# Performance work log

Measured on AMD Instinct MI355X. Metric: run time of the kernel, lower is better.

Reference implementation:

```python
import jax, jax.numpy as jnp
import numpy as np

B, L, Z, G = 512, 2713, 58, 8  # batch, chem features, seq len (zeta), d_model (gamma)
H, HD, FF, NL = 8, 1, 2048, 6  # heads, head_dim, ffn dim, layers
RNA_IN, LIN1, LIN2 = 1018, 256, 64
CAT, C1, C2 = LIN2 + Z * G, 64, 8  # 528, 64, 8


def setup_inputs() -> dict:
    key = jax.random.key(0)
    ks = iter(jax.random.split(key, 40))
    r = lambda shape, s=0.05: (jax.random.normal(next(ks), shape, dtype=jnp.float32) * s)
    inp = {
        'rna': jax.random.normal(next(ks), (B, RNA_IN), dtype=jnp.float32),
        'drug': jax.random.normal(next(ks), (B, L, Z), dtype=jnp.float32),
        'lin1_w': r((LIN1, RNA_IN)), 'lin1_b': r((LIN1,)),
        'lin2_w': r((LIN2, LIN1)), 'lin2_b': r((LIN2,)),
        'chem_w': r((G, L)),  # chem_embedding: Linear(2713->8, no bias)
        'pos_w': r((G, Z)),   # pos_embedding on one-hot == its weight columns
        'qkv_w': r((NL, 3 * G, G)), 'qkv_b': r((NL, 3 * G)),
        'out_w': r((NL, G, G)), 'out_b': r((NL, G)),
        'ln1_g': jnp.ones((NL, G), jnp.float32), 'ln1_b': jnp.zeros((NL, G), jnp.float32),
        'ff1_w': r((NL, FF, G)), 'ff1_b': r((NL, FF)),
        'ff2_w': r((NL, G, FF)), 'ff2_b': r((NL, G)),
        'ln2_g': jnp.ones((NL, G), jnp.float32), 'ln2_b': jnp.zeros((NL, G), jnp.float32),
        'c1_w': r((C1, CAT)), 'c1_b': r((C1,)),
        'c2_w': r((C2, C1)), 'c2_b': r((C2,)),
        'c3_w': r((1, C2)), 'c3_b': r((1,)),
    }
    return inp


def _layernorm(x, g, b, eps=1e-5):
    mu = jnp.mean(x, axis=-1, keepdims=True)
    var = jnp.mean(jnp.square(x - mu), axis=-1, keepdims=True)
    return (x - mu) * jax.lax.rsqrt(var + eps) * g + b


def _forward(rna, drug, lin1_w, lin1_b, lin2_w, lin2_b, chem_w, pos_w,
             qkv_w, qkv_b, out_w, out_b, ln1_g, ln1_b,
             ff1_w, ff1_b, ff2_w, ff2_b, ln2_g, ln2_b,
             c1_w, c1_b, c2_w, c2_b, c3_w, c3_b):
    # rna branch: two linear layers (no activation in original forward)
    r = rna @ lin1_w.T + lin1_b
    r = r @ lin2_w.T + lin2_b  # [B, 64]

    # Embedding: E = W_chem @ M + W_pos (the double loop, vectorized)
    E = jnp.einsum('gl,blz->bgz', chem_w, drug) + pos_w[None]  # [B, G, Z]
    x = jnp.transpose(E, (0, 2, 1))  # [B, Z, G] (batch_first transformer input)

    scale = 1.0 / np.sqrt(HD)
    for i in range(NL):  # 6 post-norm TransformerEncoderLayers, relu FFN
        qkv = x @ qkv_w[i].T + qkv_b[i]  # [B, Z, 3G]
        q, k, v = jnp.split(qkv, 3, axis=-1)
        qh = q.reshape(B, Z, H, HD)
        kh = k.reshape(B, Z, H, HD)
        vh = v.reshape(B, Z, H, HD)
        scores = jnp.einsum('bshd,bthd->bhst', qh, kh) * scale
        a = jax.nn.softmax(scores, axis=-1)
        o = jnp.einsum('bhst,bthd->bshd', a, vh).reshape(B, Z, G)
        o = o @ out_w[i].T + out_b[i]
        x = _layernorm(x + o, ln1_g[i], ln1_b[i])
        ff = jax.nn.relu(x @ ff1_w[i].T + ff1_b[i]) @ ff2_w[i].T + ff2_b[i]
        x = _layernorm(x + ff, ln2_g[i], ln2_b[i])

    flat = x.reshape(B, Z * G)  # [B, 464]
    h = jnp.concatenate([r, flat], axis=1)  # [B, 528]
    h = h @ c1_w.T + c1_b
    h = h @ c2_w.T + c2_b
    return h @ c3_w.T + c3_b  # [B, 1]


def reference(rna, drug, lin1_w, lin1_b, lin2_w, lin2_b, chem_w, pos_w,
              qkv_w, qkv_b, out_w, out_b, ln1_g, ln1_b,
              ff1_w, ff1_b, ff2_w, ff2_b, ln2_g, ln2_b,
              c1_w, c1_b, c2_w, c2_b, c3_w, c3_b):
    return _forward(rna, drug, lin1_w, lin1_b, lin2_w, lin2_b, chem_w, pos_w,
                    qkv_w, qkv_b, out_w, out_b, ln1_g, ln1_b,
                    ff1_w, ff1_b, ff2_w, ff2_b, ln2_g, ln2_b,
                    c1_w, c1_b, c2_w, c2_b, c3_w, c3_b)
```

## Files before the change

kernel.cpp:

```cpp
#include <hip/hip_runtime.h>

#define BB 512
#define LDIM 2713
#define ZDIM 58
#define GDIM 8
#define NLAYER 6
#define FFDIM 2048
#define RNAIN 1018
#define CATDIM 528
#define NCAT 1482
#define LQ 679

typedef float v2f __attribute__((ext_vector_type(2)));
typedef float f32x4 __attribute__((ext_vector_type(4)));
typedef _Float16 f16x4 __attribute__((ext_vector_type(4)));

#define OFF_WCATT  0
#define OFF_BPRIME 94848
#define OFF_W1H    94912
#define OFF_A2H    144064

__global__ __launch_bounds__(1024) void prep_kernel(
    const float* __restrict__ lin1_w, const float* __restrict__ lin1_b,
    const float* __restrict__ lin2_w, const float* __restrict__ lin2_b,
    const float* __restrict__ c1_w, const float* __restrict__ c1_b,
    const float* __restrict__ ff1_w, const float* __restrict__ ff2_w,
    float* __restrict__ ws) {
    const int t = threadIdx.x;
    const int bx = blockIdx.x;
    float* WcatT = ws + OFF_WCATT;

    if (bx >= 17) {
        int tid = (bx - 17) * 1024 + t;
        _Float16* w1hp = (_Float16*)(ws + OFF_W1H);
        _Float16* a2hp = (_Float16*)(ws + OFF_A2H);
        if (tid < NLAYER * 128 * 32) {
            int li = tid / 4096, rem = tid % 4096;
            int ft = rem >> 5, l32 = rem & 31;
            int q = l32 >> 4, i = l32 & 15;
            const float* src = ff1_w + ((size_t)li * FFDIM + ft * 16 + i) * 8 + q * 4;
            size_t dst = ((size_t)(li * 128 + ft) * 32 + l32) * 4;
            #pragma unroll
            for (int j = 0; j < 4; ++j) w1hp[dst + j] = (_Float16)src[j];
        } else {
            int r2 = tid - NLAYER * 128 * 32;
            int li = r2 / 4096, rem = r2 % 4096;
            int ft = rem >> 5, s = rem & 31;
            int q = s >> 3, i2 = s & 7;
            const float* src = ff2_w + ((size_t)li * GDIM + i2) * FFDIM + ft * 16 + q * 4;
            size_t dst = ((size_t)(li * 128 + ft) * 32 + s) * 4;
            #pragma unroll
            for (int j = 0; j < 4; ++j) a2hp[dst + j] = (_Float16)src[j];
        }
        return;
    }

    __shared__ float lin1s[256 * 64];
    __shared__ float Ut[64 * 64];
    __shared__ float c1T[64 * 64];

    if (bx == 16) {
        {
            int m = t >> 4, q = t & 15;
            float a = 0.f;
            #pragma unroll
            for (int nn = 0; nn < 16; ++nn)
                a += lin2_w[m * 256 + q * 16 + nn] * lin1_b[q * 16 + nn];
            lin1s[m * 16 + q] = a;
        }
        __syncthreads();
        if (t < 64) {
            float a = lin2_b[t];
            #pragma unroll
            for (int q = 0; q < 16; ++q) a += lin1s[t * 16 + q];
            Ut[t] = a;
        }
        __syncthreads();
        if (t < 64) {
            float a = c1_b[t];
            #pragma unroll 8
            for (int m = 0; m < 64; ++m) a += c1_w[t * CATDIM + m] * Ut[m];
            ws[OFF_BPRIME + t] = a;
        }
        for (int i = t; i < 464 * 64; i += 1024) {
            int j = i / 464, kk = i % 464;
            WcatT[(RNAIN + kk) * 64 + j] = c1_w[j * CATDIM + 64 + kk];
        }
        return;
    }

    const int k0 = bx * 64;
    const int nk = (RNAIN - k0 < 64) ? (RNAIN - k0) : 64;
    for (int i = t; i < 256 * 64; i += 1024) {
        int n = i >> 6, kl = i & 63;
        lin1s[i] = (kl < nk) ? lin1_w[n * RNAIN + k0 + kl] : 0.f;
    }
    for (int i = t; i < 64 * 64; i += 1024) {
        int j = i >> 6, m = i & 63;
        c1T[m * 64 + j] = c1_w[j * CATDIM + m];
    }
    __syncthreads();
    {
        const int kl = t & 63;
        const int mw = __builtin_amdgcn_readfirstlane(t >> 6);
        float a0 = 0.f, a1 = 0.f, a2 = 0.f, a3 = 0.f;
        for (int n = 0; n < 256; ++n) {
            float ls = lin1s[n * 64 + kl];
            a0 += lin2_w[(mw +  0) * 256 + n] * ls;
            a1 += lin2_w[(mw + 16) * 256 + n] * ls;
            a2 += lin2_w[(mw + 32) * 256 + n] * ls;
            a3 += lin2_w[(mw + 48) * 256 + n] * ls;
        }
        Ut[(mw +  0) * 64 + kl] = a0;
        Ut[(mw + 16) * 64 + kl] = a1;
        Ut[(mw + 32) * 64 + kl] = a2;
        Ut[(mw + 48) * 64 + kl] = a3;
    }
    __syncthreads();
    {
        const int j = t & 63;
        const int kw = __builtin_amdgcn_readfirstlane(t >> 6);
        float a0 = 0.f, a1 = 0.f, a2 = 0.f, a3 = 0.f;
        for (int m = 0; m < 64; ++m) {
            float cv = c1T[m * 64 + j];
            a0 += Ut[m * 64 + kw +  0] * cv;
            a1 += Ut[m * 64 + kw + 16] * cv;
            a2 += Ut[m * 64 + kw + 32] * cv;
            a3 += Ut[m * 64 + kw + 48] * cv;
        }
        if (kw +  0 < nk) WcatT[(k0 + kw +  0) * 64 + j] = a0;
        if (kw + 16 < nk) WcatT[(k0 + kw + 16) * 64 + j] = a1;
        if (kw + 32 < nk) WcatT[(k0 + kw + 32) * 64 + j] = a2;
        if (kw + 48 < nk) WcatT[(k0 + kw + 48) * 64 + j] = a3;
    }
}

__global__ __launch_bounds__(1024, 8) void mega_kernel(
    const float* __restrict__ drug, const float* __restrict__ chem_w,
    const float* __restrict__ pos_w,
    const _Float16* __restrict__ w1h, const _Float16* __restrict__ a2h,
    const float* __restrict__ ff1_b,
    const float* __restrict__ qkv_w, const float* __restrict__ qkv_b,
    const float* __restrict__ out_w, const float* __restrict__ out_b,
    const float* __restrict__ ln1_g, const float* __restrict__ ln1_b,
    const float* __restrict__ ff2_b,
    const float* __restrict__ ln2_g, const float* __restrict__ ln2_b,
    const float* __restrict__ rna, const float* __restrict__ WcatT,
    const float* __restrict__ bprime,
    const float* __restrict__ c2_w, const float* __restrict__ c2_b,
    const float* __restrict__ c3_w, const float* __restrict__ c3_b,
    float* __restrict__ out) {
    __shared__ float smem[12864];
    float* cwl    = smem;
    float* part_e = smem + 5440;
    float* xs    = smem;
    _Float16* xh = (_Float16*)(smem + 512);
    float* qs    = smem + 768;
    float* ks    = smem + 1248;
    float* vs    = smem + 1728;
    float* part  = smem + 2208;
    float* qkvws = smem + 10400;
    float* qkvbs = smem + 11552;
    float* outws = smem + 11696;
    float* outbs = smem + 12080;
    float* l1gs  = smem + 12128;
    float* l1bs  = smem + 12176;
    float* l2gs  = smem + 12224;
    float* l2bs  = smem + 12272;
    float* f2bs  = smem + 12320;
    float* h1s   = smem + 12368;
    float* h2s   = smem + 12432;

    const int b = blockIdx.x;
    const int t = threadIdx.x;
    const int w = __builtin_amdgcn_readfirstlane(t >> 6);
    const int lane = t & 63;
    const int quad = lane >> 4;
    const int i16 = lane & 15;

    {
        const int zc = (lane < ZDIM) ? lane : (ZDIM - 1);
        v2f acc0 = {0.f, 0.f}, acc1 = {0.f, 0.f}, acc2 = {0.f, 0.f}, acc3 = {0.f, 0.f};
        for (int q = 0; q < 4; ++q) {
            const int l0 = q * LQ;
            const int nrows = (LDIM - l0 < LQ) ? (LDIM - l0) : LQ;
            __syncthreads();
            #pragma unroll
            for (int gp = 0; gp < 4; ++gp)
                for (int i = t; i < nrows; i += 1024) {
                    v2f cv = { chem_w[(2 * gp) * LDIM + l0 + i],
                               chem_w[(2 * gp + 1) * LDIM + l0 + i] };
                    *(v2f*)(cwl + 2 * (gp * 680 + i)) = cv;
                }
            __syncthreads();
            const float* dp = drug + (size_t)b * (LDIM * ZDIM) + (size_t)l0 * ZDIM + zc;
            int r0 = w * 43;
            int r1 = (r0 + 43 < nrows) ? (r0 + 43) : nrows;
            int r = r0;
            for (; r + 8 <= r1; r += 8) {
                float d0 = dp[(r + 0) * ZDIM];
                float d1 = dp[(r + 1) * ZDIM];
                float d2 = dp[(r + 2) * ZDIM];
                float d3 = dp[(r + 3) * ZDIM];
                float d4 = dp[(r + 4) * ZDIM];
                float d5 = dp[(r + 5) * ZDIM];
                float d6 = dp[(r + 6) * ZDIM];
                float d7 = dp[(r + 7) * ZDIM];
                #pragma unroll
                for (int j = 0; j < 8; ++j) {
                    float dj = (j == 0) ? d0 : (j == 1) ? d1 : (j == 2) ? d2 : (j == 3) ? d3
                             : (j == 4) ? d4 : (j == 5) ? d5 : (j == 6) ? d6 : d7;
                    v2f dd = {dj, dj};
                    int rr = r + j;
                    acc0 += *(const v2f*)(cwl + 2 * (0 * 680 + rr)) * dd;
                    acc1 += *(const v2f*)(cwl + 2 * (1 * 680 + rr)) * dd;
                    acc2 += *(const v2f*)(cwl + 2 * (2 * 680 + rr)) * dd;
                    acc3 += *(const v2f*)(cwl + 2 * (3 * 680 + rr)) * dd;
                }
            }
            for (; r < r1; ++r) {
                float d = dp[r * ZDIM];
                v2f dd = {d, d};
                acc0 += *(const v2f*)(cwl + 2 * (0 * 680 + r)) * dd;
                acc1 += *(const v2f*)(cwl + 2 * (1 * 680 + r)) * dd;
                acc2 += *(const v2f*)(cwl + 2 * (2 * 680 + r)) * dd;
                acc3 += *(const v2f*)(cwl + 2 * (3 * 680 + r)) * dd;
            }
        }
        if (lane < ZDIM) {
            v2f* pr = (v2f*)(part_e + w * 464 + zc * 8);
            pr[0] = acc0; pr[1] = acc1; pr[2] = acc2; pr[3] = acc3;
        }
        __syncthreads();
        if (t < 464) {
            int z = t >> 3, g = t & 7;
            float s = pos_w[g * ZDIM + z];
            #pragma unroll
            for (int ww = 0; ww < 16; ++ww) s += part_e[ww * 464 + t];
            xs[t] = s;
        } else if (t < 512) {
            xs[t] = 0.f;
            xh[t] = (_Float16)0.f;
        }
        __syncthreads();
    }

    for (int i = t; i < 1152; i += 1024) qkvws[i] = qkv_w[i];
    if (t < 144) qkvbs[t] = qkv_b[t];
    if (t < 384) outws[t] = out_w[t];
    if (t < 48) {
        outbs[t] = out_b[t];
        l1gs[t] = ln1_g[t]; l1bs[t] = ln1_b[t];
        l2gs[t] = ln2_g[t]; l2bs[t] = ln2_b[t];
        f2bs[t] = ff2_b[t];
    }
    __syncthreads();

    for (int li = 0; li < NLAYER; ++li) {
        for (int i = t; i < 1392; i += 1024) {
            int z = i / 24, j = i - z * 24;
            const float4* xr = (const float4*)(xs + z * 8);
            float4 x0 = xr[0], x1 = xr[1];
            const float4* wr = (const float4*)(qkvws + li * 192 + j * 8);
            float4 w0 = wr[0], w1 = wr[1];
            float a = qkvbs[li * 24 + j]
                    + x0.x * w0.x + x0.y * w0.y + x0.z * w0.z + x0.w * w0.w
                    + x1.x * w1.x + x1.y * w1.y + x1.z * w1.z + x1.w * w1.w;
            int p = j >> 3, h = j & 7;
            float* dst = (p == 0) ? qs : (p == 1) ? ks : vs;
            dst[h * 60 + z] = a;
        }
        __syncthreads();

        if (t < 464) {
            int h = t & 7, s = t >> 3;
            float q = qs[h * 60 + s];
            const float4* kr = (const float4*)(ks + h * 60);
            const float4* vr = (const float4*)(vs + h * 60);
            float sum = 0.f, oa = 0.f;
            #pragma unroll 2
            for (int c = 0; c < 14; ++c) {
                float4 k4 = kr[c], v4 = vr[c];
                float e0 = __expf(q * k4.x); sum += e0; oa += e0 * v4.x;
                float e1 = __expf(q * k4.y); sum += e1; oa += e1 * v4.y;
                float e2 = __expf(q * k4.z); sum += e2; oa += e2 * v4.z;
                float e3 = __expf(q * k4.w); sum += e3; oa += e3 * v4.w;
            }
            {
                const float* kk = ks + h * 60;
                const float* vv = vs + h * 60;
                float e0 = __expf(q * kk[56]); sum += e0; oa += e0 * vv[56];
                float e1 = __expf(q * kk[57]); sum += e1; oa += e1 * vv[57];
            }
            float o = oa / sum;
            int g = h;
            float a = outbs[li * 8 + g] + xs[t];
            const float* wr8 = outws + li * 64 + g * 8;
            #pragma unroll
            for (int hh = 0; hh < 8; ++hh)
                a += __shfl(o, hh, 8) * wr8[hh];
            float s8 = a + __shfl_xor(a, 1);
            s8 += __shfl_xor(s8, 2);
            s8 += __shfl_xor(s8, 4);
            float mu = s8 * 0.125f;
            float d = a - mu;
            float vv = d * d;
            vv += __shfl_xor(vv, 1); vv += __shfl_xor(vv, 2); vv += __shfl_xor(vv, 4);
            float inv = rsqrtf(vv * 0.125f + 1e-5f);
            float xn = d * inv * l1gs[li * 8 + g] + l1bs[li * 8 + g];
            xs[t] = xn;
            xh[t] = (_Float16)xn;
        }
        __syncthreads();

        {
            f16x4 xb[4];
            #pragma unroll
            for (int nt = 0; nt < 4; ++nt) {
                if (quad < 2) {
                    xb[nt] = *(const f16x4*)(xh + (nt * 16 + i16) * 8 + quad * 4);
                } else {
                    xb[nt][0] = (_Float16)0.f; xb[nt][1] = (_Float16)0.f;
                    xb[nt][2] = (_Float16)0.f; xb[nt][3] = (_Float16)0.f;
                }
            }
            f32x4 oacc[4];
            #pragma unroll
            for (int nt = 0; nt < 4; ++nt) { oacc[nt][0]=0.f; oacc[nt][1]=0.f; oacc[nt][2]=0.f; oacc[nt][3]=0.f; }

            const _Float16* w1p = w1h + ((size_t)(li * 128 + w * 8) * 32) * 4;
            const _Float16* a2p = a2h + ((size_t)(li * 128 + w * 8) * 32) * 4;
            const float* b1p = ff1_b + li * FFDIM + w * 128;

            #pragma unroll
            for (int ft = 0; ft < 8; ++ft) {
                f16x4 w1f = {};
                if (lane < 32) w1f = *(const f16x4*)(w1p + (size_t)(ft * 32 + lane) * 4);
                f16x4 a2f = {};
                if (i16 < 8) a2f = *(const f16x4*)(a2p + (size_t)(ft * 32 + quad * 8 + i16) * 4);
                f32x4 b1v = *(const f32x4*)(b1p + ft * 16 + quad * 4);
                #pragma unroll
                for (int nt = 0; nt < 4; ++nt) {
                    f32x4 h = __builtin_amdgcn_mfma_f32_16x16x16f16(w1f, xb[nt], b1v, 0, 0, 0);
                    h[0] = fmaxf(h[0], 0.f); h[1] = fmaxf(h[1], 0.f);
                    h[2] = fmaxf(h[2], 0.f); h[3] = fmaxf(h[3], 0.f);
                    f16x4 hb;
                    hb[0] = (_Float16)h[0]; hb[1] = (_Float16)h[1];
                    hb[2] = (_Float16)h[2]; hb[3] = (_Float16)h[3];
                    oacc[nt] = __builtin_amdgcn_mfma_f32_16x16x16f16(a2f, hb, oacc[nt], 0, 0, 0);
                }
            }
            if (quad < 2) {
                #pragma unroll
                for (int nt = 0; nt < 4; ++nt) {
                    float4 o4 = make_float4(oacc[nt][0], oacc[nt][1], oacc[nt][2], oacc[nt][3]);
                    *(float4*)(part + ((w * 64 + nt * 16 + i16) * 8 + quad * 4)) = o4;
                }
            }
        }
        __syncthreads();

        if (t < 464) {
            int z = t >> 3, g = t & 7;
            float s = 0.f;
            #pragma unroll
            for (int ww = 0; ww < 16; ++ww) s += part[(ww * 64 + z) * 8 + g];
            float a = xs[t] + s + f2bs[li * 8 + g];
            float s8 = a + __shfl_xor(a, 1);
            s8 += __shfl_xor(s8, 2);
            s8 += __shfl_xor(s8, 4);
            float mu = s8 * 0.125f;
            float d = a - mu;
            float vv = d * d;
            vv += __shfl_xor(vv, 1); vv += __shfl_xor(vv, 2); vv += __shfl_xor(vv, 4);
            float inv = rsqrtf(vv * 0.125f + 1e-5f);
            xs[t] = d * inv * l2gs[li * 8 + g] + l2bs[li * 8 + g];
        }
        __syncthreads();
    }

    {
        float* cat = part;
        float* partial = part + 2048;
        const float* rg = rna + (size_t)b * RNAIN;
        for (int i = t; i < RNAIN; i += 1024) cat[i] = rg[i];
        __syncthreads();
        int j = lane;
        int k0 = w * 93;
        int k1 = (k0 + 93 < NCAT) ? (k0 + 93) : NCAT;
        float a = (w == 0) ? bprime[j] : 0.f;
        #pragma unroll 4
        for (int k = k0; k < k1; ++k) {
            float ck = (k < RNAIN) ? cat[k] : xs[k - RNAIN];
            a += ck * WcatT[k * 64 + j];
        }
        partial[w * 64 + j] = a;
        __syncthreads();
        if (t < 64) {
            float s = 0.f;
            #pragma unroll
            for (int ww = 0; ww < 16; ++ww) s += partial[ww * 64 + t];
            h1s[t] = s;
        }
    }
    __syncthreads();
    if (t < 8) {
        float a2 = c2_b[t];
        #pragma unroll 8
        for (int m = 0; m < 64; ++m) a2 += h1s[m] * c2_w[t * 64 + m];
        h2s[t] = a2;
    }
    __syncthreads();
    if (t == 0) {
        float a3 = c3_b[0];
        #pragma unroll
        for (int jj = 0; jj < 8; ++jj) a3 += h2s[jj] * c3_w[jj];
        out[b] = a3;
    }
}

extern "C" void kernel_launch(void* const* d_in, const int* in_sizes, int n_in,
                              void* d_out, int out_size, void* d_ws, size_t ws_size,
                              hipStream_t stream) {
    const float* rna    = (const float*)d_in[0];
    const float* drug   = (const float*)d_in[1];
    const float* lin1_w = (const float*)d_in[2];
    const float* lin1_b = (const float*)d_in[3];
    const float* lin2_w = (const float*)d_in[4];
    const float* lin2_b = (const float*)d_in[5];
    const float* chem_w = (const float*)d_in[6];
    const float* pos_w  = (const float*)d_in[7];
    const float* qkv_w  = (const float*)d_in[8];
    const float* qkv_b  = (const float*)d_in[9];
    const float* out_w  = (const float*)d_in[10];
    const float* out_b  = (const float*)d_in[11];
    const float* ln1_g  = (const float*)d_in[12];
    const float* ln1_b  = (const float*)d_in[13];
    const float* ff1_w  = (const float*)d_in[14];
    const float* ff1_b  = (const float*)d_in[15];
    const float* ff2_w  = (const float*)d_in[16];
    const float* ff2_b  = (const float*)d_in[17];
    const float* ln2_g  = (const float*)d_in[18];
    const float* ln2_b  = (const float*)d_in[19];
    const float* c1_w   = (const float*)d_in[20];
    const float* c1_b   = (const float*)d_in[21];
    const float* c2_w   = (const float*)d_in[22];
    const float* c2_b   = (const float*)d_in[23];
    const float* c3_w   = (const float*)d_in[24];
    const float* c3_b   = (const float*)d_in[25];
    float* ws  = (float*)d_ws;
    float* out = (float*)d_out;

    hipLaunchKernelGGL(prep_kernel, dim3(65), dim3(1024), 0, stream,
                       lin1_w, lin1_b, lin2_w, lin2_b, c1_w, c1_b, ff1_w, ff2_w, ws);
    hipLaunchKernelGGL(mega_kernel, dim3(BB), dim3(1024), 0, stream,
                       drug, chem_w, pos_w,
                       (const _Float16*)(ws + OFF_W1H), (const _Float16*)(ws + OFF_A2H),
                       ff1_b, qkv_w, qkv_b, out_w, out_b,
                       ln1_g, ln1_b, ff2_b, ln2_g, ln2_b,
                       rna, ws + OFF_WCATT, ws + OFF_BPRIME,
                       c2_w, c2_b, c3_w, c3_b, out);
}
```

Before: 650.7 us.

## Transpose chem weights in prep kernel and read them from global in embedding

Adds a prep block that transposes chem_w into an [L,8] layout in workspace. The embedding stage no longer stages chem weights through shared memory in four chunks with barriers. Instead each wave covers a contiguous 170-row slice and reads the transposed weights with wave-uniform float4 global loads. This removes the shared-memory staging and the __syncthreads between chunks, but relies on cache hits for the weight reads and changes how rows are split across waves.

```diff
diff --git a/kernel.cpp b/kernel.cpp
--- a/kernel.cpp
+++ b/kernel.cpp
@@ -9,7 +9,6 @@
 #define RNAIN 1018
 #define CATDIM 528
 #define NCAT 1482
-#define LQ 679
 
 typedef float v2f __attribute__((ext_vector_type(2)));
 typedef float f32x4 __attribute__((ext_vector_type(4)));
@@ -19,16 +18,27 @@
 #define OFF_BPRIME 94848
 #define OFF_W1H    94912
 #define OFF_A2H    144064
+#define OFF_CHEMT  193216
 
 __global__ __launch_bounds__(1024) void prep_kernel(
     const float* __restrict__ lin1_w, const float* __restrict__ lin1_b,
     const float* __restrict__ lin2_w, const float* __restrict__ lin2_b,
     const float* __restrict__ c1_w, const float* __restrict__ c1_b,
     const float* __restrict__ ff1_w, const float* __restrict__ ff2_w,
+    const float* __restrict__ chem_w,
     float* __restrict__ ws) {
     const int t = threadIdx.x;
     const int bx = blockIdx.x;
     float* WcatT = ws + OFF_WCATT;
+
+    if (bx == 65) {
+        float* chemT = ws + OFF_CHEMT;
+        #pragma unroll
+        for (int g = 0; g < 8; ++g)
+            for (int l = t; l < LDIM; l += 1024)
+                chemT[l * 8 + g] = chem_w[g * LDIM + l];
+        return;
+    }
 
     if (bx >= 17) {
         int tid = (bx - 17) * 1024 + t;
@@ -136,7 +146,7 @@
 }
 
 __global__ __launch_bounds__(1024, 8) void mega_kernel(
-    const float* __restrict__ drug, const float* __restrict__ chem_w,
+    const float* __restrict__ drug, const float* __restrict__ chemT,
     const float* __restrict__ pos_w,
     const _Float16* __restrict__ w1h, const _Float16* __restrict__ a2h,
     const float* __restrict__ ff1_b,
@@ -151,7 +161,6 @@
     const float* __restrict__ c3_w, const float* __restrict__ c3_b,
     float* __restrict__ out) {
     __shared__ float smem[12864];
-    float* cwl    = smem;
     float* part_e = smem + 5440;
     float* xs    = smem;
     _Float16* xh = (_Float16*)(smem + 512);
@@ -180,56 +189,36 @@
 
     {
         const int zc = (lane < ZDIM) ? lane : (ZDIM - 1);
-        v2f acc0 = {0.f, 0.f}, acc1 = {0.f, 0.f}, acc2 = {0.f, 0.f}, acc3 = {0.f, 0.f};
-        for (int q = 0; q < 4; ++q) {
-            const int l0 = q * LQ;
-            const int nrows = (LDIM - l0 < LQ) ? (LDIM - l0) : LQ;
-            __syncthreads();
-            #pragma unroll
-            for (int gp = 0; gp < 4; ++gp)
-                for (int i = t; i < nrows; i += 1024) {
-                    v2f cv = { chem_w[(2 * gp) * LDIM + l0 + i],
-                               chem_w[(2 * gp + 1) * LDIM + l0 + i] };
-                    *(v2f*)(cwl + 2 * (gp * 680 + i)) = cv;
-                }
-            __syncthreads();
-            const float* dp = drug + (size_t)b * (LDIM * ZDIM) + (size_t)l0 * ZDIM + zc;
-            int r0 = w * 43;
-            int r1 = (r0 + 43 < nrows) ? (r0 + 43) : nrows;
-            int r = r0;
-            for (; r + 8 <= r1; r += 8) {
-                float d0 = dp[(r + 0) * ZDIM];
-                float d1 = dp[(r + 1) * ZDIM];
-                float d2 = dp[(r + 2) * ZDIM];
-                float d3 = dp[(r + 3) * ZDIM];
-                float d4 = dp[(r + 4) * ZDIM];
-                float d5 = dp[(r + 5) * ZDIM];
-                float d6 = dp[(r + 6) * ZDIM];
-                float d7 = dp[(r + 7) * ZDIM];
-                #pragma unroll
-                for (int j = 0; j < 8; ++j) {
-                    float dj = (j == 0) ? d0 : (j == 1) ? d1 : (j == 2) ? d2 : (j == 3) ? d3
-                             : (j == 4) ? d4 : (j == 5) ? d5 : (j == 6) ? d6 : d7;
-                    v2f dd = {dj, dj};
-                    int rr = r + j;
-                    acc0 += *(const v2f*)(cwl + 2 * (0 * 680 + rr)) * dd;
-                    acc1 += *(const v2f*)(cwl + 2 * (1 * 680 + rr)) * dd;
-                    acc2 += *(const v2f*)(cwl + 2 * (2 * 680 + rr)) * dd;
-                    acc3 += *(const v2f*)(cwl + 2 * (3 * 680 + rr)) * dd;
-                }
-            }
-            for (; r < r1; ++r) {
-                float d = dp[r * ZDIM];
-                v2f dd = {d, d};
-                acc0 += *(const v2f*)(cwl + 2 * (0 * 680 + r)) * dd;
-                acc1 += *(const v2f*)(cwl + 2 * (1 * 680 + r)) * dd;
-                acc2 += *(const v2f*)(cwl + 2 * (2 * 680 + r)) * dd;
-                acc3 += *(const v2f*)(cwl + 2 * (3 * 680 + r)) * dd;
-            }
+        const float* dp = drug + (size_t)b * (LDIM * ZDIM) + zc;
+        int r0 = w * 170;
+        int r1 = (r0 + 170 < LDIM) ? (r0 + 170) : LDIM;
+        f32x4 accA = {0.f, 0.f, 0.f, 0.f}, accB = {0.f, 0.f, 0.f, 0.f};
+        int r = r0;
+        for (; r + 4 <= r1; r += 4) {
+            float d0 = dp[(size_t)(r + 0) * ZDIM];
+            float d1 = dp[(size_t)(r + 1) * ZDIM];
+            float d2 = dp[(size_t)(r + 2) * ZDIM];
+            float d3 = dp[(size_t)(r + 3) * ZDIM];
+            const f32x4* c0 = (const f32x4*)(chemT + (r + 0) * 8);
+            const f32x4* c1 = (const f32x4*)(chemT + (r + 1) * 8);
+            const f32x4* c2 = (const f32x4*)(chemT + (r + 2) * 8);
+            const f32x4* c3 = (const f32x4*)(chemT + (r + 3) * 8);
+            f32x4 dd;
+            dd = (f32x4){d0, d0, d0, d0}; accA += c0[0] * dd; accB += c0[1] * dd;
+            dd = (f32x4){d1, d1, d1, d1}; accA += c1[0] * dd; accB += c1[1] * dd;
+            dd = (f32x4){d2, d2, d2, d2}; accA += c2[0] * dd; accB += c2[1] * dd;
+            dd = (f32x4){d3, d3, d3, d3}; accA += c3[0] * dd; accB += c3[1] * dd;
+        }
+        for (; r < r1; ++r) {
+            float d = dp[(size_t)r * ZDIM];
+            const f32x4* cc = (const f32x4*)(chemT + r * 8);
+            f32x4 dd = {d, d, d, d};
+            accA += cc[0] * dd; accB += cc[1] * dd;
         }
         if (lane < ZDIM) {
-            v2f* pr = (v2f*)(part_e + w * 464 + zc * 8);
-            pr[0] = acc0; pr[1] = acc1; pr[2] = acc2; pr[3] = acc3;
+            float4* pr = (float4*)(part_e + w * 464 + zc * 8);
+            pr[0] = make_float4(accA[0], accA[1], accA[2], accA[3]);
+            pr[1] = make_float4(accB[0], accB[1], accB[2], accB[3]);
         }
         __syncthreads();
         if (t < 464) {
@@ -451,10 +440,11 @@
     float* ws  = (float*)d_ws;
     float* out = (float*)d_out;
 
-    hipLaunchKernelGGL(prep_kernel, dim3(65), dim3(1024), 0, stream,
-                       lin1_w, lin1_b, lin2_w, lin2_b, c1_w, c1_b, ff1_w, ff2_w, ws);
+    hipLaunchKernelGGL(prep_kernel, dim3(66), dim3(1024), 0, stream,
+                       lin1_w, lin1_b, lin2_w, lin2_b, c1_w, c1_b, ff1_w, ff2_w,
+                       chem_w, ws);
     hipLaunchKernelGGL(mega_kernel, dim3(BB), dim3(1024), 0, stream,
-                       drug, chem_w, pos_w,
+                       drug, ws + OFF_CHEMT, pos_w,
                        (const _Float16*)(ws + OFF_W1H), (const _Float16*)(ws + OFF_A2H),
                        ff1_b, qkv_w, qkv_b, out_w, out_b,
                        ln1_g, ln1_b, ff2_b, ln2_g, ln2_b,
```

After: 649.0 us. About the same (-0.3%).
